# Kernel tuning notes

Measured on AMD Instinct MI355X. Metric: run time of the kernel, lower is better.

## Reference

```python
import jax, jax.numpy as jnp
import numpy as np


def gcn_conv(x, W, src, dst, edge_weight, n_nodes):
    """PyG GCNConv (bias=False, add_self_loops=True, normalize=True).
    out = D^{-1/2} (A + I) D^{-1/2} X W, with deg computed from edge weights
    into each destination node plus the self-loop weight 1.
    """
    h = x @ W  # [N, F_out]
    deg = jax.ops.segment_sum(edge_weight, dst, num_segments=n_nodes) + 1.0  # self-loop w=1
    dinv = jax.lax.rsqrt(deg)  # deg >= 1 so safe
    norm = dinv[src] * edge_weight * dinv[dst]  # [E]
    # gather -> weight -> scatter-add
    agg = jax.ops.segment_sum(norm[:, None] * h[src], dst, num_segments=n_nodes)
    # self-loop contribution: norm_ii = deg_i^{-1}
    return agg + h * (1.0 / deg)[:, None]


def setup_inputs() -> dict:
    key = jax.random.key(0)
    k1, k2, k3, k4, k5 = jax.random.split(key, 5)
    N, E = 10000, 160000
    in_ch, hidden, out_ch = 512, 512, 256
    x = jax.random.normal(k1, (N, in_ch), dtype=jnp.float32)
    edge_index = jax.random.randint(k2, (2, E), 0, N, dtype=jnp.int64)
    edge_weight = jax.random.uniform(k3, (E,), dtype=jnp.float32)
    # Glorot-style init like torch_geometric.nn.dense.linear
    W1 = jax.random.normal(k4, (in_ch, hidden), dtype=jnp.float32) * (1.0 / np.sqrt(in_ch))
    W2 = jax.random.normal(k5, (hidden, out_ch), dtype=jnp.float32) * (1.0 / np.sqrt(hidden))
    return {"x": x, "edge_index": edge_index, "edge_weight": edge_weight, "W1": W1, "W2": W2}


def reference(x, edge_index, edge_weight, W1, W2):
    n_nodes = x.shape[0]
    src, dst = edge_index[0], edge_index[1]
    h = jax.nn.relu(gcn_conv(x, W1, src, dst, edge_weight, n_nodes))
    # dropout is identity in eval mode
    return gcn_conv(h, W2, src, dst, edge_weight, n_nodes)
```

## Files before the change

kernel.cpp:

```cpp
#include <hip/hip_runtime.h>

#define N_NODES 10000
#define N_EDGES 160000
#define M_PAD   10112
#define MT      79
#define KT      8
#define ELLW    64

typedef short s8v __attribute__((ext_vector_type(8)));
typedef short s4v __attribute__((ext_vector_type(4)));
typedef float f4v __attribute__((ext_vector_type(4)));

__device__ inline short f2bf(float f) {
    unsigned u = __builtin_bit_cast(unsigned, f);
    u += 0x7FFF + ((u >> 16) & 1);
    return (short)(u >> 16);
}
__device__ inline float bf2f(short s) {
    return __builtin_bit_cast(float, ((unsigned)(unsigned short)s) << 16);
}

#define GLD_LDS16(g, l)                                                      \
    __builtin_amdgcn_global_load_lds(                                        \
        (const __attribute__((address_space(1))) unsigned int*)(g),          \
        (__attribute__((address_space(3))) unsigned int*)(l), 16, 0, 0)

__global__ __launch_bounds__(256) void k_prep(const float* __restrict__ x,
                                              const float* __restrict__ W1,
                                              const float* __restrict__ W2,
                                              char* __restrict__ x_bf,
                                              char* __restrict__ w1T,
                                              char* __restrict__ w2T,
                                              float* __restrict__ deg,
                                              int* __restrict__ count) {
    int bid = blockIdx.x;
    if (bid < 2528) {
        long long t = (long long)bid * 256 + threadIdx.x;
        int gr = (int)(t >> 6);
        int c  = (int)(t & 63);
        s8v v;
        if (gr < N_NODES) {
            const float* p = &x[(long long)gr * 512 + c * 8];
#pragma unroll
            for (int j = 0; j < 8; j++) v[j] = f2bf(p[j]);
        } else {
#pragma unroll
            for (int j = 0; j < 8; j++) v[j] = 0;
        }
        int r = gr & 127, tm = gr >> 7, tk = c >> 3, sc = c & 7;
        int slot = sc ^ (r & 7);
        *(s8v*)&x_bf[(((long long)tm * KT + tk) << 14) + r * 128 + slot * 16] = v;
    } else if (bid < 2720) {
        const float* W;
        char* out;
        int ncols, t;
        if (bid < 2656) { W = W1; out = w1T; ncols = 512; t = (bid - 2528) * 256 + threadIdx.x; }
        else            { W = W2; out = w2T; ncols = 256; t = (bid - 2656) * 256 + threadIdx.x; }
        int n = t >> 6;
        int c = t & 63;
        s8v v;
#pragma unroll
        for (int j = 0; j < 8; j++) v[j] = f2bf(W[(long long)(c * 8 + j) * ncols + n]);
        int r = n & 127, tn = n >> 7, tk = c >> 3, sc = c & 7;
        int slot = sc ^ (r & 7);
        *(s8v*)&out[(((long long)tn * KT + tk) << 14) + r * 128 + slot * 16] = v;
    } else {
        int i = (bid - 2720) * 256 + threadIdx.x;
        if (i < N_NODES) { deg[i] = 1.0f; count[i] = 0; }
    }
}

__device__ __forceinline__ void gemm_block(const char* __restrict__ ga,
                                           const char* __restrict__ gb,
                                           short* __restrict__ Cb,
                                           int M, int N, int row_blk, int col_blk,
                                           char* As, char* Bs) {
    int tid = threadIdx.x, lane = tid & 63, w = tid >> 6;
    int wr = w >> 1, wc = w & 1;

    f4v acc[4][4];
#pragma unroll
    for (int m = 0; m < 4; m++)
#pragma unroll
        for (int n = 0; n < 4; n++) acc[m][n] = (f4v){0.f, 0.f, 0.f, 0.f};

    for (int kt = 0; kt < KT; ++kt) {
        const char* a0 = ga + (kt << 14);
        const char* b0 = gb + (kt << 14);
#pragma unroll
        for (int j = 0; j < 4; ++j) {
            int off = (j * 256 + w * 64) * 16;
            GLD_LDS16(a0 + off + lane * 16, As + off);
            GLD_LDS16(b0 + off + lane * 16, Bs + off);
        }
        __syncthreads();

#pragma unroll
        for (int kk = 0; kk < 2; ++kk) {
            s8v a[4], b[4];
#pragma unroll
            for (int m = 0; m < 4; ++m) {
                int r = wr * 64 + m * 16 + (lane & 15);
                int slot = ((lane >> 4) + kk * 4) ^ (r & 7);
                a[m] = *(const s8v*)&As[r * 128 + slot * 16];
            }
#pragma unroll
            for (int n = 0; n < 4; ++n) {
                int r = wc * 64 + n * 16 + (lane & 15);
                int slot = ((lane >> 4) + kk * 4) ^ (r & 7);
                b[n] = *(const s8v*)&Bs[r * 128 + slot * 16];
            }
#pragma unroll
            for (int m = 0; m < 4; ++m)
#pragma unroll
                for (int n = 0; n < 4; ++n)
                    acc[m][n] = __builtin_amdgcn_mfma_f32_16x16x32_bf16(a[m], b[n], acc[m][n], 0, 0, 0);
        }
        __syncthreads();
    }

    int row0 = row_blk * 128 + wr * 64;
    int col0 = col_blk * 128 + wc * 64;
#pragma unroll
    for (int m = 0; m < 4; ++m) {
#pragma unroll
        for (int q = 0; q < 4; ++q) {
            int row = row0 + m * 16 + (lane >> 4) * 4 + q;
            if (row < M) {
#pragma unroll
                for (int n = 0; n < 4; ++n) {
                    int col = col0 + n * 16 + (lane & 15);
                    Cb[(long long)row * N + col] = f2bf(acc[m][n][q]);
                }
            }
        }
    }
}

__global__ __launch_bounds__(256) void k_gemm1_deg(const char* __restrict__ A,
                                                   const char* __restrict__ B,
                                                   short* __restrict__ Cb,
                                                   const int* __restrict__ src,
                                                   const int* __restrict__ dst,
                                                   const float* __restrict__ wgt,
                                                   float* __restrict__ deg,
                                                   int* __restrict__ count,
                                                   int2* __restrict__ ell) {
    int bid = blockIdx.x;
    if (bid >= 316) {
        int e = (bid - 316) * 256 + threadIdx.x;
        if (e < N_EDGES) {
            int d = dst[e];
            float wv = wgt[e];
            atomicAdd(&deg[d], wv);
            int pos = atomicAdd(&count[d], 1);
            if (pos < ELLW)
                ell[(long long)d * ELLW + pos] = make_int2(src[e], __float_as_int(wv));
        }
        return;
    }
    __shared__ char As[16384];
    __shared__ char Bs[16384];
    int bx = bid & 3, by = bid >> 2;
    gemm_block(A + ((long long)by * KT << 14), B + ((long long)bx * KT << 14),
               Cb, N_NODES, 512, by, bx, As, Bs);
}

__global__ __launch_bounds__(256) void k_gemm_bf16(const char* __restrict__ A,
                                                   const char* __restrict__ B,
                                                   short* __restrict__ Cb,
                                                   int M, int N) {
    __shared__ char As[16384];
    __shared__ char Bs[16384];
    gemm_block(A + ((long long)blockIdx.y * KT << 14),
               B + ((long long)blockIdx.x * KT << 14),
               Cb, M, N, blockIdx.y, blockIdx.x, As, Bs);
}

template <int F, bool RELU, bool OUT_TILED>
__global__ __launch_bounds__(256) void k_gather(const int2* __restrict__ ell,
                                                const int* __restrict__ count,
                                                const short* __restrict__ hb,
                                                const float* __restrict__ deg,
                                                void* __restrict__ outp,
                                                int n_waves) {
    const int FPT = F / 64;
    int wave = (int)((blockIdx.x * (long long)blockDim.x + threadIdx.x) >> 6);
    if (wave >= n_waves) return;
    int lane = threadIdx.x & 63;

    float acc[FPT];
#pragma unroll
    for (int j = 0; j < FPT; j++) acc[j] = 0.f;

    if (wave < N_NODES) {
        float dg = deg[wave];
        float inv = 1.0f / dg;
        float dinv_d = rsqrtf(dg);
        {
            if constexpr (FPT == 8) {
                s8v v = *(const s8v*)&hb[(long long)wave * F + lane * 8];
#pragma unroll
                for (int j = 0; j < 8; j++) acc[j] = bf2f(v[j]) * inv;
            } else {
                s4v v = *(const s4v*)&hb[(long long)wave * F + lane * 4];
#pragma unroll
                for (int j = 0; j < 4; j++) acc[j] = bf2f(v[j]) * inv;
            }
        }
        int cnt = count[wave];
        if (cnt > ELLW) cnt = ELLW;
        const int2* row = &ell[(long long)wave * ELLW];
        int p = 0;
        for (; p + 3 < cnt; p += 4) {
            int2 e0 = row[p], e1 = row[p + 1], e2 = row[p + 2], e3 = row[p + 3];
            float n0 = rsqrtf(deg[e0.x]) * __int_as_float(e0.y) * dinv_d;
            float n1 = rsqrtf(deg[e1.x]) * __int_as_float(e1.y) * dinv_d;
            float n2 = rsqrtf(deg[e2.x]) * __int_as_float(e2.y) * dinv_d;
            float n3 = rsqrtf(deg[e3.x]) * __int_as_float(e3.y) * dinv_d;
            if constexpr (FPT == 8) {
                s8v v0 = *(const s8v*)&hb[(long long)e0.x * F + lane * 8];
                s8v v1 = *(const s8v*)&hb[(long long)e1.x * F + lane * 8];
                s8v v2 = *(const s8v*)&hb[(long long)e2.x * F + lane * 8];
                s8v v3 = *(const s8v*)&hb[(long long)e3.x * F + lane * 8];
#pragma unroll
                for (int j = 0; j < 8; j++)
                    acc[j] += n0 * bf2f(v0[j]) + n1 * bf2f(v1[j]) + n2 * bf2f(v2[j]) + n3 * bf2f(v3[j]);
            } else {
                s4v v0 = *(const s4v*)&hb[(long long)e0.x * F + lane * 4];
                s4v v1 = *(const s4v*)&hb[(long long)e1.x * F + lane * 4];
                s4v v2 = *(const s4v*)&hb[(long long)e2.x * F + lane * 4];
                s4v v3 = *(const s4v*)&hb[(long long)e3.x * F + lane * 4];
#pragma unroll
                for (int j = 0; j < 4; j++)
                    acc[j] += n0 * bf2f(v0[j]) + n1 * bf2f(v1[j]) + n2 * bf2f(v2[j]) + n3 * bf2f(v3[j]);
            }
        }
        for (; p < cnt; ++p) {
            int2 e0 = row[p];
            float n0 = rsqrtf(deg[e0.x]) * __int_as_float(e0.y) * dinv_d;
            if constexpr (FPT == 8) {
                s8v v0 = *(const s8v*)&hb[(long long)e0.x * F + lane * 8];
#pragma unroll
                for (int j = 0; j < 8; j++) acc[j] += n0 * bf2f(v0[j]);
            } else {
                s4v v0 = *(const s4v*)&hb[(long long)e0.x * F + lane * 4];
#pragma unroll
                for (int j = 0; j < 4; j++) acc[j] += n0 * bf2f(v0[j]);
            }
        }
        if (RELU) {
#pragma unroll
            for (int j = 0; j < FPT; j++) acc[j] = fmaxf(acc[j], 0.f);
        }
    }

    if constexpr (OUT_TILED) {
        s8v v;
#pragma unroll
        for (int j = 0; j < 8; j++) v[j] = f2bf(acc[j]);
        int tm = wave >> 7, r = wave & 127, tk = lane >> 3, sc = lane & 7;
        int slot = sc ^ (r & 7);
        char* out = (char*)outp;
        *(s8v*)&out[(((long long)tm * KT + tk) << 14) + r * 128 + slot * 16] = v;
    } else {
        float* out = (float*)outp + (long long)wave * F + lane * FPT;
#pragma unroll
        for (int j = 0; j < FPT; j += 4) {
            *(float4*)&out[j] = make_float4(acc[j], acc[j + 1], acc[j + 2], acc[j + 3]);
        }
    }
}

extern "C" void kernel_launch(void* const* d_in, const int* in_sizes, int n_in,
                              void* d_out, int out_size, void* d_ws, size_t ws_size,
                              hipStream_t stream) {
    const float* x  = (const float*)d_in[0];
    const int*   ei = (const int*)d_in[1];
    const float* w  = (const float*)d_in[2];
    const float* W1 = (const float*)d_in[3];
    const float* W2 = (const float*)d_in[4];
    float* out = (float*)d_out;

    const int* src = ei;
    const int* dst = ei + N_EDGES;

    char* p = (char*)d_ws;
    auto alloc = [&](size_t bytes) {
        char* r = p;
        p += (bytes + 255) & ~(size_t)255;
        return r;
    };
    char*  x_bf   = alloc((size_t)MT * KT * 16384);
    char*  a1_bf  = alloc((size_t)MT * KT * 16384);
    char*  w1T    = alloc((size_t)4 * KT * 16384);
    char*  w2T    = alloc((size_t)2 * KT * 16384);
    short* h1_bf  = (short*)alloc((size_t)N_NODES * 512 * 2);
    short* h2_bf  = (short*)alloc((size_t)N_NODES * 256 * 2);
    float* deg    = (float*)alloc(N_NODES * 4);
    int*   count  = (int*)alloc(N_NODES * 4);
    int2*  ell    = (int2*)alloc((size_t)N_NODES * ELLW * 8);

    const int B = 256;

    k_prep<<<2760, B, 0, stream>>>(x, W1, W2, x_bf, w1T, w2T, deg, count);
    k_gemm1_deg<<<316 + 625, B, 0, stream>>>(x_bf, w1T, h1_bf, src, dst, w, deg, count, ell);
    k_gather<512, true, true><<<(M_PAD * 64) / B, B, 0, stream>>>(
        ell, count, h1_bf, deg, a1_bf, M_PAD);
    k_gemm_bf16<<<dim3(2, MT), B, 0, stream>>>(a1_bf, w2T, h2_bf, N_NODES, 256);
    k_gather<256, false, false><<<(N_NODES * 64) / B, B, 0, stream>>>(
        ell, count, h2_bf, deg, out, N_NODES);
}
```

Before: 91.67 us.

## Fuse x bf16 conversion into GEMM1, remap blocks across XCDs, retile GEMM2

The separate pass that converted x to a swizzled bf16 layout is removed. GEMM1 now loads fp32 x directly, converts it in registers and writes it into LDS, which saves a full write and read of the converted activation buffer. Both GEMMs use a block-to-tile mapping meant to group row tiles per XCD for better L2 reuse of shared operands. GEMM2 switches to 128x64 tiles so it launches 320 blocks instead of 158 and fills more CUs. The cost is that GEMM1's A loads are now synchronous register loads instead of direct-to-LDS loads, and fp32 reads are wider and are repeated for each of the 4 column blocks.

```diff
diff --git a/kernel.cpp b/kernel.cpp
--- a/kernel.cpp
+++ b/kernel.cpp
@@ -25,37 +25,19 @@
         (const __attribute__((address_space(1))) unsigned int*)(g),          \
         (__attribute__((address_space(3))) unsigned int*)(l), 16, 0, 0)
 
-__global__ __launch_bounds__(256) void k_prep(const float* __restrict__ x,
-                                              const float* __restrict__ W1,
+__global__ __launch_bounds__(256) void k_prep(const float* __restrict__ W1,
                                               const float* __restrict__ W2,
-                                              char* __restrict__ x_bf,
                                               char* __restrict__ w1T,
                                               char* __restrict__ w2T,
                                               float* __restrict__ deg,
                                               int* __restrict__ count) {
     int bid = blockIdx.x;
-    if (bid < 2528) {
-        long long t = (long long)bid * 256 + threadIdx.x;
-        int gr = (int)(t >> 6);
-        int c  = (int)(t & 63);
-        s8v v;
-        if (gr < N_NODES) {
-            const float* p = &x[(long long)gr * 512 + c * 8];
-#pragma unroll
-            for (int j = 0; j < 8; j++) v[j] = f2bf(p[j]);
-        } else {
-#pragma unroll
-            for (int j = 0; j < 8; j++) v[j] = 0;
-        }
-        int r = gr & 127, tm = gr >> 7, tk = c >> 3, sc = c & 7;
-        int slot = sc ^ (r & 7);
-        *(s8v*)&x_bf[(((long long)tm * KT + tk) << 14) + r * 128 + slot * 16] = v;
-    } else if (bid < 2720) {
+    if (bid < 192) {
         const float* W;
         char* out;
         int ncols, t;
-        if (bid < 2656) { W = W1; out = w1T; ncols = 512; t = (bid - 2528) * 256 + threadIdx.x; }
-        else            { W = W2; out = w2T; ncols = 256; t = (bid - 2656) * 256 + threadIdx.x; }
+        if (bid < 128) { W = W1; out = w1T; ncols = 512; t = bid * 256 + threadIdx.x; }
+        else           { W = W2; out = w2T; ncols = 256; t = (bid - 128) * 256 + threadIdx.x; }
         int n = t >> 6;
         int c = t & 63;
         s8v v;
@@ -65,80 +47,18 @@
         int slot = sc ^ (r & 7);
         *(s8v*)&out[(((long long)tn * KT + tk) << 14) + r * 128 + slot * 16] = v;
     } else {
-        int i = (bid - 2720) * 256 + threadIdx.x;
+        int i = (bid - 192) * 256 + threadIdx.x;
         if (i < N_NODES) { deg[i] = 1.0f; count[i] = 0; }
     }
 }
 
-__device__ __forceinline__ void gemm_block(const char* __restrict__ ga,
-                                           const char* __restrict__ gb,
-                                           short* __restrict__ Cb,
-                                           int M, int N, int row_blk, int col_blk,
-                                           char* As, char* Bs) {
-    int tid = threadIdx.x, lane = tid & 63, w = tid >> 6;
-    int wr = w >> 1, wc = w & 1;
-
-    f4v acc[4][4];
-#pragma unroll
-    for (int m = 0; m < 4; m++)
-#pragma unroll
-        for (int n = 0; n < 4; n++) acc[m][n] = (f4v){0.f, 0.f, 0.f, 0.f};
-
-    for (int kt = 0; kt < KT; ++kt) {
-        const char* a0 = ga + (kt << 14);
-        const char* b0 = gb + (kt << 14);
-#pragma unroll
-        for (int j = 0; j < 4; ++j) {
-            int off = (j * 256 + w * 64) * 16;
-            GLD_LDS16(a0 + off + lane * 16, As + off);
-            GLD_LDS16(b0 + off + lane * 16, Bs + off);
-        }
-        __syncthreads();
-
-#pragma unroll
-        for (int kk = 0; kk < 2; ++kk) {
-            s8v a[4], b[4];
-#pragma unroll
-            for (int m = 0; m < 4; ++m) {
-                int r = wr * 64 + m * 16 + (lane & 15);
-                int slot = ((lane >> 4) + kk * 4) ^ (r & 7);
-                a[m] = *(const s8v*)&As[r * 128 + slot * 16];
-            }
-#pragma unroll
-            for (int n = 0; n < 4; ++n) {
-                int r = wc * 64 + n * 16 + (lane & 15);
-                int slot = ((lane >> 4) + kk * 4) ^ (r & 7);
-                b[n] = *(const s8v*)&Bs[r * 128 + slot * 16];
-            }
-#pragma unroll
-            for (int m = 0; m < 4; ++m)
-#pragma unroll
-                for (int n = 0; n < 4; ++n)
-                    acc[m][n] = __builtin_amdgcn_mfma_f32_16x16x32_bf16(a[m], b[n], acc[m][n], 0, 0, 0);
-        }
-        __syncthreads();
-    }
-
-    int row0 = row_blk * 128 + wr * 64;
-    int col0 = col_blk * 128 + wc * 64;
-#pragma unroll
-    for (int m = 0; m < 4; ++m) {
-#pragma unroll
-        for (int q = 0; q < 4; ++q) {
-            int row = row0 + m * 16 + (lane >> 4) * 4 + q;
-            if (row < M) {
-#pragma unroll
-                for (int n = 0; n < 4; ++n) {
-                    int col = col0 + n * 16 + (lane & 15);
-                    Cb[(long long)row * N + col] = f2bf(acc[m][n][q]);
-                }
-            }
-        }
-    }
-}
-
-__global__ __launch_bounds__(256) void k_gemm1_deg(const char* __restrict__ A,
-                                                   const char* __restrict__ B,
+__device__ __forceinline__ void xcd_map(int b, int& by, int& bx) {
+    by = (b & 7) * 10 + ((b >> 3) >> 2);
+    bx = (b >> 3) & 3;
+}
+
+__global__ __launch_bounds__(256) void k_gemm1_deg(const float* __restrict__ x,
+                                                   const char* __restrict__ w1T,
                                                    short* __restrict__ Cb,
                                                    const int* __restrict__ src,
                                                    const int* __restrict__ dst,
@@ -147,8 +67,8 @@
                                                    int* __restrict__ count,
                                                    int2* __restrict__ ell) {
     int bid = blockIdx.x;
-    if (bid >= 316) {
-        int e = (bid - 316) * 256 + threadIdx.x;
+    if (bid >= 320) {
+        int e = (bid - 320) * 256 + threadIdx.x;
         if (e < N_EDGES) {
             int d = dst[e];
             float wv = wgt[e];
@@ -159,22 +79,162 @@
         }
         return;
     }
+    int by, bx;
+    xcd_map(bid, by, bx);
+    if (by >= MT) return;
+
     __shared__ char As[16384];
     __shared__ char Bs[16384];
-    int bx = bid & 3, by = bid >> 2;
-    gemm_block(A + ((long long)by * KT << 14), B + ((long long)bx * KT << 14),
-               Cb, N_NODES, 512, by, bx, As, Bs);
-}
-
-__global__ __launch_bounds__(256) void k_gemm_bf16(const char* __restrict__ A,
-                                                   const char* __restrict__ B,
-                                                   short* __restrict__ Cb,
-                                                   int M, int N) {
+    int tid = threadIdx.x, lane = tid & 63, w = tid >> 6;
+    int wr = w >> 1, wc = w & 1;
+
+    const char* gb = w1T + ((long long)bx * KT << 14);
+
+    f4v acc[4][4];
+#pragma unroll
+    for (int m = 0; m < 4; m++)
+#pragma unroll
+        for (int n = 0; n < 4; n++) acc[m][n] = (f4v){0.f, 0.f, 0.f, 0.f};
+
+    for (int kt = 0; kt < KT; ++kt) {
+#pragma unroll
+        for (int it = 0; it < 8; ++it) {
+            int c = it * 256 + tid;
+            int r = c >> 4, f4 = c & 15;
+            int gr = by * 128 + r;
+            float4 v = make_float4(0.f, 0.f, 0.f, 0.f);
+            if (gr < N_NODES) v = *(const float4*)&x[(long long)gr * 512 + kt * 64 + f4 * 4];
+            s4v b;
+            b[0] = f2bf(v.x); b[1] = f2bf(v.y); b[2] = f2bf(v.z); b[3] = f2bf(v.w);
+            int slot = (f4 >> 1) ^ (r & 7);
+            *(s4v*)&As[r * 128 + slot * 16 + (f4 & 1) * 8] = b;
+        }
+        const char* b0 = gb + (kt << 14);
+#pragma unroll
+        for (int j = 0; j < 4; ++j) {
+            int off = (j * 256 + w * 64) * 16;
+            GLD_LDS16(b0 + off + lane * 16, Bs + off);
+        }
+        __syncthreads();
+
+#pragma unroll
+        for (int kk = 0; kk < 2; ++kk) {
+            s8v a[4], b[4];
+#pragma unroll
+            for (int m = 0; m < 4; ++m) {
+                int r = wr * 64 + m * 16 + (lane & 15);
+                int slot = ((lane >> 4) + kk * 4) ^ (r & 7);
+                a[m] = *(const s8v*)&As[r * 128 + slot * 16];
+            }
+#pragma unroll
+            for (int n = 0; n < 4; ++n) {
+                int r = wc * 64 + n * 16 + (lane & 15);
+                int slot = ((lane >> 4) + kk * 4) ^ (r & 7);
+                b[n] = *(const s8v*)&Bs[r * 128 + slot * 16];
+            }
+#pragma unroll
+            for (int m = 0; m < 4; ++m)
+#pragma unroll
+                for (int n = 0; n < 4; ++n)
+                    acc[m][n] = __builtin_amdgcn_mfma_f32_16x16x32_bf16(a[m], b[n], acc[m][n], 0, 0, 0);
+        }
+        __syncthreads();
+    }
+
+    int row0 = by * 128 + wr * 64;
+    int col0 = bx * 128 + wc * 64;
+#pragma unroll
+    for (int m = 0; m < 4; ++m) {
+#pragma unroll
+        for (int q = 0; q < 4; ++q) {
+            int row = row0 + m * 16 + (lane >> 4) * 4 + q;
+            if (row < N_NODES) {
+#pragma unroll
+                for (int n = 0; n < 4; ++n) {
+                    int col = col0 + n * 16 + (lane & 15);
+                    Cb[(long long)row * 512 + col] = f2bf(acc[m][n][q]);
+                }
+            }
+        }
+    }
+}
+
+__global__ __launch_bounds__(256) void k_gemm2(const char* __restrict__ A,
+                                               const char* __restrict__ w2T,
+                                               short* __restrict__ Cb) {
+    int by, bx;
+    xcd_map(blockIdx.x, by, bx);
+    if (by >= MT) return;
+
     __shared__ char As[16384];
-    __shared__ char Bs[16384];
-    gemm_block(A + ((long long)blockIdx.y * KT << 14),
-               B + ((long long)blockIdx.x * KT << 14),
-               Cb, M, N, blockIdx.y, blockIdx.x, As, Bs);
+    __shared__ char Bs[8192];
+    int tid = threadIdx.x, lane = tid & 63, w = tid >> 6;
+    int wr = w >> 1, wc = w & 1;
+
+    const char* ga = A + ((long long)by * KT << 14);
+    const char* gbase = w2T + ((long long)(bx >> 1) * KT << 14) + (bx & 1) * 8192;
+
+    f4v acc[4][2];
+#pragma unroll
+    for (int m = 0; m < 4; m++)
+#pragma unroll
+        for (int n = 0; n < 2; n++) acc[m][n] = (f4v){0.f, 0.f, 0.f, 0.f};
+
+    for (int kt = 0; kt < KT; ++kt) {
+        const char* a0 = ga + (kt << 14);
+        const char* b0 = gbase + (kt << 14);
+#pragma unroll
+        for (int j = 0; j < 4; ++j) {
+            int off = (j * 256 + w * 64) * 16;
+            GLD_LDS16(a0 + off + lane * 16, As + off);
+        }
+#pragma unroll
+        for (int j = 0; j < 2; ++j) {
+            int off = (j * 256 + w * 64) * 16;
+            GLD_LDS16(b0 + off + lane * 16, Bs + off);
+        }
+        __syncthreads();
+
+#pragma unroll
+        for (int kk = 0; kk < 2; ++kk) {
+            s8v a[4], b[2];
+#pragma unroll
+            for (int m = 0; m < 4; ++m) {
+                int r = wr * 64 + m * 16 + (lane & 15);
+                int slot = ((lane >> 4) + kk * 4) ^ (r & 7);
+                a[m] = *(const s8v*)&As[r * 128 + slot * 16];
+            }
+#pragma unroll
+            for (int n = 0; n < 2; ++n) {
+                int r = wc * 32 + n * 16 + (lane & 15);
+                int slot = ((lane >> 4) + kk * 4) ^ (r & 7);
+                b[n] = *(const s8v*)&Bs[r * 128 + slot * 16];
+            }
+#pragma unroll
+            for (int m = 0; m < 4; ++m)
+#pragma unroll
+                for (int n = 0; n < 2; ++n)
+                    acc[m][n] = __builtin_amdgcn_mfma_f32_16x16x32_bf16(a[m], b[n], acc[m][n], 0, 0, 0);
+        }
+        __syncthreads();
+    }
+
+    int row0 = by * 128 + wr * 64;
+    int col0 = bx * 64 + wc * 32;
+#pragma unroll
+    for (int m = 0; m < 4; ++m) {
+#pragma unroll
+        for (int q = 0; q < 4; ++q) {
+            int row = row0 + m * 16 + (lane >> 4) * 4 + q;
+            if (row < N_NODES) {
+#pragma unroll
+                for (int n = 0; n < 2; ++n) {
+                    int col = col0 + n * 16 + (lane & 15);
+                    Cb[(long long)row * 256 + col] = f2bf(acc[m][n][q]);
+                }
+            }
+        }
+    }
 }
 
 template <int F, bool RELU, bool OUT_TILED>
@@ -291,7 +351,6 @@
         p += (bytes + 255) & ~(size_t)255;
         return r;
     };
-    char*  x_bf   = alloc((size_t)MT * KT * 16384);
     char*  a1_bf  = alloc((size_t)MT * KT * 16384);
     char*  w1T    = alloc((size_t)4 * KT * 16384);
     char*  w2T    = alloc((size_t)2 * KT * 16384);
@@ -303,11 +362,11 @@
 
     const int B = 256;
 
-    k_prep<<<2760, B, 0, stream>>>(x, W1, W2, x_bf, w1T, w2T, deg, count);
-    k_gemm1_deg<<<316 + 625, B, 0, stream>>>(x_bf, w1T, h1_bf, src, dst, w, deg, count, ell);
+    k_prep<<<232, B, 0, stream>>>(W1, W2, w1T, w2T, deg, count);
+    k_gemm1_deg<<<320 + 625, B, 0, stream>>>(x, w1T, h1_bf, src, dst, w, deg, count, ell);
     k_gather<512, true, true><<<(M_PAD * 64) / B, B, 0, stream>>>(
         ell, count, h1_bf, deg, a1_bf, M_PAD);
-    k_gemm_bf16<<<dim3(2, MT), B, 0, stream>>>(a1_bf, w2T, h2_bf, N_NODES, 256);
+    k_gemm2<<<320, B, 0, stream>>>(a1_bf, w2T, h2_bf);
     k_gather<256, false, false><<<(N_NODES * 64) / B, B, 0, stream>>>(
         ell, count, h2_bf, deg, out, N_NODES);
 }
```

Result: slower. 102.0 us (+11.3%).
